# Optimization experiments

Hardware: AMD Instinct MI355X
Metric: run time of the kernel (lower is better)

## Reference

```python
import jax, jax.numpy as jnp
import numpy as np


def gcn_conv(x, W, b, src, dst, dinv_sqrt, n_nodes):
    # PyG GCNConv: h = X W; out_i = sum_j norm_ij * h_j + b, norm = d_i^-1/2 d_j^-1/2
    h = x @ W  # [N, out]
    norm = dinv_sqrt[src] * dinv_sqrt[dst]  # [E]
    msg = h[src] * norm[:, None]  # [E, out]
    out = jax.ops.segment_sum(msg, dst, num_segments=n_nodes)
    return out + b


def setup_inputs() -> dict:
    key = jax.random.key(0)
    ks = jax.random.split(key, 12)
    N, E, G = 50000, 400000, 512
    x = jax.random.normal(ks[0], (N, 3), dtype=jnp.float32)
    edge_index = jax.random.randint(ks[1], (2, E), 0, N, dtype=jnp.int64)
    batch = jnp.sort(jax.random.randint(ks[2], (N,), 0, G, dtype=jnp.int64))
    def lin(k, fin, fout):
        kw, kb = jax.random.split(k)
        s = 1.0 / np.sqrt(fin)
        return (jax.random.uniform(kw, (fin, fout), jnp.float32, -s, s),
                jax.random.uniform(kb, (fout,), jnp.float32, -s, s))
    W1, b1 = lin(ks[3], 3, 100)
    W2, b2 = lin(ks[4], 100, 200)
    W3, b3 = lin(ks[5], 200, 100)
    W4, b4 = lin(ks[6], 100, 1)
    return {"x": x, "edge_index": edge_index, "batch": batch, "num_graphs": G,
            "W1": W1, "b1": b1, "W2": W2, "b2": b2,
            "W3": W3, "b3": b3, "W4": W4, "b4": b4}


def reference(x, edge_index, batch, num_graphs, W1, b1, W2, b2, W3, b3, W4, b4):
    N = x.shape[0]
    loop = jnp.arange(N, dtype=edge_index.dtype)
    src = jnp.concatenate([edge_index[0], loop])  # self-loops added (GCNConv default)
    dst = jnp.concatenate([edge_index[1], loop])
    deg = jax.ops.segment_sum(jnp.ones_like(src, dtype=x.dtype), dst, num_segments=N)
    dinv_sqrt = deg ** -0.5  # deg >= 1 due to self-loops

    h = jax.nn.silu(gcn_conv(x, W1, b1, src, dst, dinv_sqrt, N))
    h = jax.nn.silu(gcn_conv(h, W2, b2, src, dst, dinv_sqrt, N))

    # global_mean_pool over `batch` segments
    sums = jax.ops.segment_sum(h, batch, num_segments=num_graphs)  # [G, 200]
    cnts = jax.ops.segment_sum(jnp.ones((N,), h.dtype), batch, num_segments=num_graphs)
    pooled = sums / jnp.maximum(cnts, 1.0)[:, None]

    h = jax.nn.silu(pooled @ W3 + b3)
    out = h @ W4 + b4  # [G, 1]
    return out.squeeze(-1)
```

## Files before the change

### kernel.cpp

```cpp
#include <hip/hip_runtime.h>
#include <math.h>

#define WF 64

__device__ __forceinline__ float silu_f(float v){ return v / (1.0f + expf(-v)); }

__global__ __launch_bounds__(256) void k_count(const int* __restrict__ dst, int* __restrict__ cnt, int E){
  int e = blockIdx.x*blockDim.x + threadIdx.x;
  if (e < E) atomicAdd(&cnt[dst[e]], 1);
}

__global__ __launch_bounds__(256) void k_scan1(const int* __restrict__ cnt, int* __restrict__ rowstart, int* __restrict__ bsum, int N){
  __shared__ int s[256];
  int tid = threadIdx.x;
  int base = blockIdx.x*2048 + tid*8;
  int loc[8]; int tsum = 0;
#pragma unroll
  for (int j=0;j<8;++j){ int idx=base+j; int v = (idx<N)?cnt[idx]:0; loc[j]=tsum; tsum+=v; }
  s[tid]=tsum; __syncthreads();
  for (int off=1; off<256; off<<=1){
    int v = (tid>=off)? s[tid-off] : 0;
    __syncthreads();
    s[tid] += v;
    __syncthreads();
  }
  int texc = s[tid] - tsum;
  if (tid==255) bsum[blockIdx.x] = s[255];
#pragma unroll
  for (int j=0;j<8;++j){ int idx=base+j; if (idx<N) rowstart[idx] = texc + loc[j]; }
}

__global__ __launch_bounds__(256) void k_scan3(const int* __restrict__ bsum, const int* __restrict__ cnt,
                        const float* __restrict__ x,
                        int* __restrict__ rowstart, int* __restrict__ cursor,
                        float* __restrict__ dinv, float4* __restrict__ dxp,
                        int N, int E, int nb){
  __shared__ int boffs;
  int tid = threadIdx.x;
  int b = (blockIdx.x*blockDim.x) >> 11;
  if (tid < WF){
    int v = (tid < nb && tid < b) ? bsum[tid] : 0;
#pragma unroll
    for (int off=32; off; off>>=1) v += __shfl_down(v, off);
    if (tid==0) boffs = v;
  }
  __syncthreads();
  int idx = blockIdx.x*blockDim.x + tid;
  if (idx < N){
    int v = rowstart[idx] + boffs;
    rowstart[idx]=v; cursor[idx]=v;
    float di = rsqrtf((float)(cnt[idx]+1));
    dinv[idx] = di;
    float4 o;
    o.x = di;
    o.y = di*x[3*idx+0];
    o.z = di*x[3*idx+1];
    o.w = di*x[3*idx+2];
    dxp[idx] = o;
  }
  if (idx==0) rowstart[N]=E;
}

__global__ __launch_bounds__(256) void k_fill(const int* __restrict__ src, const int* __restrict__ dst,
                       int* __restrict__ cursor, int* __restrict__ colsrc, int E){
  int e = blockIdx.x*blockDim.x + threadIdx.x;
  if (e < E){
    int d = dst[e];
    int pos = atomicAdd(&cursor[d], 1);
    colsrc[pos] = src[e];
  }
}

__global__ __launch_bounds__(256) void k_l1(const float4* __restrict__ dxp,
                     const int* __restrict__ rowstart, const int* __restrict__ colsrc,
                     const float* __restrict__ W1, const float* __restrict__ b1,
                     float* __restrict__ h1s, int N){
  __shared__ float w[300];
  __shared__ float bb[100];
  int tid = threadIdx.x;
  for (int t=tid; t<300; t+=blockDim.x) w[t]=W1[t];
  for (int t=tid; t<100; t+=blockDim.x) bb[t]=b1[t];
  __syncthreads();
  int i = blockIdx.x*blockDim.x + tid;
  if (i >= N) return;
  float4 self = dxp[i];
  float di = self.x;
  float sx = self.y, sy = self.z, sz = self.w;
  int jb = rowstart[i], je = rowstart[i+1];
  int j = jb;
  for (; j+3 < je; j += 4){
    float4 r0 = dxp[colsrc[j]];
    float4 r1 = dxp[colsrc[j+1]];
    float4 r2 = dxp[colsrc[j+2]];
    float4 r3 = dxp[colsrc[j+3]];
    sx += (r0.y + r1.y) + (r2.y + r3.y);
    sy += (r0.z + r1.z) + (r2.z + r3.z);
    sz += (r0.w + r1.w) + (r2.w + r3.w);
  }
  for (; j < je; ++j){
    float4 r = dxp[colsrc[j]];
    sx += r.y; sy += r.z; sz += r.w;
  }
  sx*=di; sy*=di; sz*=di;
  float* orow = h1s + (size_t)i*100;
#pragma unroll
  for (int f0=0; f0<100; f0+=4){
    float4 o;
    o.x = silu_f(sx*w[f0+0] + sy*w[100+f0+0] + sz*w[200+f0+0] + bb[f0+0]);
    o.y = silu_f(sx*w[f0+1] + sy*w[100+f0+1] + sz*w[200+f0+1] + bb[f0+1]);
    o.z = silu_f(sx*w[f0+2] + sy*w[100+f0+2] + sz*w[200+f0+2] + bb[f0+2]);
    o.w = silu_f(sx*w[f0+3] + sy*w[100+f0+3] + sz*w[200+f0+3] + bb[f0+3]);
    *(float4*)&orow[f0] = o;
  }
}

__global__ __launch_bounds__(256) void k_agg2(const float* __restrict__ h1s, const int* __restrict__ rowstart,
                       const int* __restrict__ colsrc, const float* __restrict__ dinv,
                       float* __restrict__ a2, int N){
  int node = blockIdx.x*8 + (threadIdx.x >> 5);
  int lane = threadIdx.x & 31;
  if (node >= N) return;
  bool act = lane < 25;
  float di = dinv[node];
  float4 acc = make_float4(0.f,0.f,0.f,0.f);
  if (act){
    float4 v = *(const float4*)(h1s + (size_t)node*100 + lane*4);
    acc.x = di*v.x; acc.y = di*v.y; acc.z = di*v.z; acc.w = di*v.w;
  }
  int jb = rowstart[node], je = rowstart[node+1];
  int j = jb;
  for (; j+1 < je; j += 2){
    int u0 = colsrc[j];   float w0 = dinv[u0];
    int u1 = colsrc[j+1]; float w1 = dinv[u1];
    if (act){
      float4 r0 = *(const float4*)(h1s + (size_t)u0*100 + lane*4);
      float4 r1 = *(const float4*)(h1s + (size_t)u1*100 + lane*4);
      acc.x += w0*r0.x + w1*r1.x;
      acc.y += w0*r0.y + w1*r1.y;
      acc.z += w0*r0.z + w1*r1.z;
      acc.w += w0*r0.w + w1*r1.w;
    }
  }
  if (j < je){
    int u = colsrc[j]; float wv = dinv[u];
    if (act){
      float4 r = *(const float4*)(h1s + (size_t)u*100 + lane*4);
      acc.x += wv*r.x; acc.y += wv*r.y; acc.z += wv*r.z; acc.w += wv*r.w;
    }
  }
  if (act){
    float4 o;
    o.x = di*acc.x; o.y = di*acc.y; o.z = di*acc.z; o.w = di*acc.w;
    *(float4*)(a2 + (size_t)node*100 + lane*4) = o;
  }
}

#define CH 20
__global__ __launch_bounds__(256, 2) void k_mm2(const float* __restrict__ a2, const float* __restrict__ W2,
                      const float* __restrict__ b2, const int* __restrict__ batch,
                      float* __restrict__ pooled, int N){
  __shared__ float aS[CH][260];
  __shared__ float wS[100][48];
  int tid = threadIdx.x;
  int fg = tid & 3;
  int ng = tid >> 2;
  int n0 = blockIdx.x * 256;
  int fb = blockIdx.y;

  for (int idx = tid; idx < 4000; idx += 256){
    int k = idx / 40, f = idx - k*40;
    int g = f / 10, j = f - g*10;
    wS[k][g*12 + j] = W2[(size_t)k*200 + fb*40 + f];
  }

  float acc[4][10];
#pragma unroll
  for (int i=0;i<4;++i)
#pragma unroll
    for (int j=0;j<10;++j) acc[i][j]=0.f;

  int gn = n0 + tid;
  bool inb = (gn < N);
  const float* arow = a2 + (size_t)gn*100;

  for (int kc = 0; kc < 5; ++kc){
    int kt = kc*CH;
    __syncthreads();
#pragma unroll
    for (int c = 0; c < 5; ++c){
      float4 v = make_float4(0.f,0.f,0.f,0.f);
      if (inb) v = *(const float4*)(arow + kt + c*4);
      aS[c*4+0][tid] = v.x;
      aS[c*4+1][tid] = v.y;
      aS[c*4+2][tid] = v.z;
      aS[c*4+3][tid] = v.w;
    }
    __syncthreads();
#pragma unroll
    for (int kl = 0; kl < CH; ++kl){
      float a[4], w[10];
      *(float4*)a = *(const float4*)&aS[kl][ng*4];
      const float* wr = &wS[kt+kl][fg*12];
      *(float4*)&w[0] = *(const float4*)&wr[0];
      *(float4*)&w[4] = *(const float4*)&wr[4];
      *(float2*)&w[8] = *(const float2*)&wr[8];
#pragma unroll
      for (int j=0;j<10;++j){
        float wv = w[j];
#pragma unroll
        for (int i=0;i<4;++i) acc[i][j] += a[i]*wv;
      }
    }
  }

  float* plL = &aS[0][0];
  __syncthreads();
  for (int idx = tid; idx < 640; idx += 256) plL[idx] = 0.f;
  __syncthreads();

  int fbase = fb*40 + fg*10;
  float bias[10];
#pragma unroll
  for (int j=0;j<10;++j) bias[j] = b2[fbase+j];
  int g0 = batch[n0];
  float s[10];
  int gprev = -1;
#pragma unroll
  for (int i=0;i<4;++i){
    int n = n0 + ng*4 + i;
    if (n < N){
      int g = batch[n];
      if (g != gprev){
        if (gprev >= 0){
          int dg = gprev - g0;
          if (dg < 16){
#pragma unroll
            for (int j=0;j<10;++j) atomicAdd(&plL[dg*40 + fg*10 + j], s[j]);
          } else {
#pragma unroll
            for (int j=0;j<10;++j) atomicAdd(&pooled[(size_t)gprev*200 + fbase + j], s[j]);
          }
        }
        gprev = g;
#pragma unroll
        for (int j=0;j<10;++j) s[j] = 0.f;
      }
#pragma unroll
      for (int j=0;j<10;++j) s[j] += silu_f(acc[i][j] + bias[j]);
    }
  }
  if (gprev >= 0){
    int dg = gprev - g0;
    if (dg < 16){
#pragma unroll
      for (int j=0;j<10;++j) atomicAdd(&plL[dg*40 + fg*10 + j], s[j]);
    } else {
#pragma unroll
      for (int j=0;j<10;++j) atomicAdd(&pooled[(size_t)gprev*200 + fbase + j], s[j]);
    }
  }
  __syncthreads();
  for (int idx = tid; idx < 640; idx += 256){
    float v = plL[idx];
    if (v != 0.f){
      int r = idx / 40, f = idx - r*40;
      atomicAdd(&pooled[(size_t)(g0+r)*200 + fb*40 + f], v);
    }
  }
}

__global__ __launch_bounds__(256) void k_head(const float* __restrict__ pooled, const int* __restrict__ batch,
                       const float* __restrict__ W3, const float* __restrict__ b3,
                       const float* __restrict__ W4, const float* __restrict__ b4,
                       float* __restrict__ out, int N){
  __shared__ float pl[200];
  __shared__ float h3[100];
  int g = blockIdx.x; int tid = threadIdx.x;
  int lo=0, hi=N;
  while (lo<hi){ int m=(lo+hi)>>1; if (batch[m] < g) lo=m+1; else hi=m; }
  int s = lo;
  hi=N;
  while (lo<hi){ int m=(lo+hi)>>1; if (batch[m] < g+1) lo=m+1; else hi=m; }
  int e = lo;
  float inv = (e>s) ? 1.0f/(float)(e-s) : 0.0f;
  if (tid < 200) pl[tid] = pooled[(size_t)g*200 + tid] * inv;
  __syncthreads();
  if (tid < 100){
    float acc = b3[tid];
    for (int k=0;k<200;++k) acc += pl[k]*W3[k*100+tid];
    h3[tid] = silu_f(acc);
  }
  __syncthreads();
  if (tid < WF){
    float p = 0.f;
    if (tid < 100)      p  = h3[tid]     * W4[tid];
    if (tid + 64 < 100) p += h3[tid+64]  * W4[tid+64];
#pragma unroll
    for (int off=32; off; off>>=1) p += __shfl_down(p, off);
    if (tid==0) out[g] = p + b4[0];
  }
}

extern "C" void kernel_launch(void* const* d_in, const int* in_sizes, int n_in,
                              void* d_out, int out_size, void* d_ws, size_t ws_size,
                              hipStream_t stream){
  const float* x  = (const float*)d_in[0];
  const int*   ei = (const int*)  d_in[1];
  const int* batch= (const int*)  d_in[2];
  const float* W1 = (const float*)d_in[4];
  const float* b1 = (const float*)d_in[5];
  const float* W2 = (const float*)d_in[6];
  const float* b2 = (const float*)d_in[7];
  const float* W3 = (const float*)d_in[8];
  const float* b3 = (const float*)d_in[9];
  const float* W4 = (const float*)d_in[10];
  const float* b4 = (const float*)d_in[11];
  float* out = (float*)d_out;

  int N = in_sizes[0]/3;
  int E = in_sizes[1]/2;
  int G = out_size;
  const int* src = ei;
  const int* dst = ei + E;

  char* base = (char*)d_ws; size_t off = 0;
  auto alloc = [&](size_t bytes)->void*{
    void* p = base + off;
    off = (off + bytes + 255) & ~(size_t)255;
    return p;
  };
  int*   cnt      = (int*)  alloc((size_t)N*4);
  float* pooled   = (float*)alloc((size_t)G*200*4);
  size_t zbytes   = off;
  int*   rowstart = (int*)  alloc((size_t)(N+1)*4);
  int*   cursor   = (int*)  alloc((size_t)N*4);
  int*   bsum     = (int*)  alloc(4096);
  int*   colsrc   = (int*)  alloc((size_t)E*4);
  float* dinv     = (float*)alloc((size_t)N*4);
  float4* dxp     = (float4*)alloc((size_t)N*16);
  float* h1s      = (float*)alloc((size_t)N*100*4);
  float* a2       = (float*)alloc((size_t)N*100*4);
  (void)ws_size; (void)n_in;

  hipMemsetAsync(base, 0, zbytes, stream);
  int gE = (E+255)/256;
  k_count<<<gE,256,0,stream>>>(dst, cnt, E);
  int nb = (N+2047)/2048;
  k_scan1<<<nb,256,0,stream>>>(cnt, rowstart, bsum, N);
  k_scan3<<<(N+255)/256,256,0,stream>>>(bsum, cnt, x, rowstart, cursor, dinv, dxp, N, E, nb);
  k_fill<<<gE,256,0,stream>>>(src, dst, cursor, colsrc, E);
  k_l1<<<(N+255)/256,256,0,stream>>>(dxp, rowstart, colsrc, W1, b1, h1s, N);
  k_agg2<<<(N+7)/8,256,0,stream>>>(h1s, rowstart, colsrc, dinv, a2, N);
  dim3 gmm((N+255)/256, 5);
  k_mm2<<<gmm,256,0,stream>>>(a2, W2, b2, batch, pooled, N);
  k_head<<<G,256,0,stream>>>(pooled, batch, W3, b3, W4, b4, out, N);
}
```

Before: 184.2 us.

## Shrink mm2 node tile to 128 and stream W2 chunks per k-step

Reworks the layer-2 matmul+pool kernel to use 128-node tiles with 2 rows per thread instead of 256 nodes with 4. W2 is now loaded per 20-row k-chunk rather than all at once, which cuts shared memory and registers. The grid is transposed so the 5 feature blocks sharing a node tile launch next to each other, which should improve L2 reuse of a2. The aim is more blocks and higher occupancy, at the cost of less register reuse per W load and more loads and syncs.

```diff
diff --git a/kernel.cpp b/kernel.cpp
--- a/kernel.cpp
+++ b/kernel.cpp
@@ -156,66 +156,62 @@
 }
 
 #define CH 20
-__global__ __launch_bounds__(256, 2) void k_mm2(const float* __restrict__ a2, const float* __restrict__ W2,
+__global__ __launch_bounds__(256) void k_mm2(const float* __restrict__ a2, const float* __restrict__ W2,
                       const float* __restrict__ b2, const int* __restrict__ batch,
                       float* __restrict__ pooled, int N){
-  __shared__ float aS[CH][260];
-  __shared__ float wS[100][48];
+  __shared__ float aS[CH][132];
+  __shared__ float wS[CH][48];
   int tid = threadIdx.x;
   int fg = tid & 3;
   int ng = tid >> 2;
-  int n0 = blockIdx.x * 256;
-  int fb = blockIdx.y;
-
-  for (int idx = tid; idx < 4000; idx += 256){
-    int k = idx / 40, f = idx - k*40;
-    int g = f / 10, j = f - g*10;
-    wS[k][g*12 + j] = W2[(size_t)k*200 + fb*40 + f];
-  }
-
-  float acc[4][10];
-#pragma unroll
-  for (int i=0;i<4;++i)
+  int fb = blockIdx.x;
+  int n0 = blockIdx.y * 128;
+
+  float acc[2][10];
+#pragma unroll
+  for (int i=0;i<2;++i)
 #pragma unroll
     for (int j=0;j<10;++j) acc[i][j]=0.f;
-
-  int gn = n0 + tid;
-  bool inb = (gn < N);
-  const float* arow = a2 + (size_t)gn*100;
 
   for (int kc = 0; kc < 5; ++kc){
     int kt = kc*CH;
     __syncthreads();
-#pragma unroll
-    for (int c = 0; c < 5; ++c){
+    for (int idx = tid; idx < 640; idx += 256){
+      int n = idx / 5, q = idx - n*5;
+      int gn = n0 + n;
       float4 v = make_float4(0.f,0.f,0.f,0.f);
-      if (inb) v = *(const float4*)(arow + kt + c*4);
-      aS[c*4+0][tid] = v.x;
-      aS[c*4+1][tid] = v.y;
-      aS[c*4+2][tid] = v.z;
-      aS[c*4+3][tid] = v.w;
+      if (gn < N) v = *(const float4*)(a2 + (size_t)gn*100 + kt + q*4);
+      aS[q*4+0][n] = v.x;
+      aS[q*4+1][n] = v.y;
+      aS[q*4+2][n] = v.z;
+      aS[q*4+3][n] = v.w;
+    }
+    for (int idx = tid; idx < 800; idx += 256){
+      int kl = idx / 40, f = idx - kl*40;
+      int g = f / 10, j = f - g*10;
+      wS[kl][g*12 + j] = W2[(size_t)(kt+kl)*200 + fb*40 + f];
     }
     __syncthreads();
 #pragma unroll
     for (int kl = 0; kl < CH; ++kl){
-      float a[4], w[10];
-      *(float4*)a = *(const float4*)&aS[kl][ng*4];
-      const float* wr = &wS[kt+kl][fg*12];
+      float a[2], w[10];
+      *(float2*)a = *(const float2*)&aS[kl][ng*2];
+      const float* wr = &wS[kl][fg*12];
       *(float4*)&w[0] = *(const float4*)&wr[0];
       *(float4*)&w[4] = *(const float4*)&wr[4];
       *(float2*)&w[8] = *(const float2*)&wr[8];
 #pragma unroll
       for (int j=0;j<10;++j){
         float wv = w[j];
-#pragma unroll
-        for (int i=0;i<4;++i) acc[i][j] += a[i]*wv;
+        acc[0][j] += a[0]*wv;
+        acc[1][j] += a[1]*wv;
       }
     }
   }
 
   float* plL = &aS[0][0];
   __syncthreads();
-  for (int idx = tid; idx < 640; idx += 256) plL[idx] = 0.f;
+  for (int idx = tid; idx < 320; idx += 256) plL[idx] = 0.f;
   __syncthreads();
 
   int fbase = fb*40 + fg*10;
@@ -226,14 +222,14 @@
   float s[10];
   int gprev = -1;
 #pragma unroll
-  for (int i=0;i<4;++i){
-    int n = n0 + ng*4 + i;
+  for (int i=0;i<2;++i){
+    int n = n0 + ng*2 + i;
     if (n < N){
       int g = batch[n];
       if (g != gprev){
         if (gprev >= 0){
           int dg = gprev - g0;
-          if (dg < 16){
+          if (dg < 8){
 #pragma unroll
             for (int j=0;j<10;++j) atomicAdd(&plL[dg*40 + fg*10 + j], s[j]);
           } else {
@@ -251,7 +247,7 @@
   }
   if (gprev >= 0){
     int dg = gprev - g0;
-    if (dg < 16){
+    if (dg < 8){
 #pragma unroll
       for (int j=0;j<10;++j) atomicAdd(&plL[dg*40 + fg*10 + j], s[j]);
     } else {
@@ -260,7 +256,7 @@
     }
   }
   __syncthreads();
-  for (int idx = tid; idx < 640; idx += 256){
+  for (int idx = tid; idx < 320; idx += 256){
     float v = plL[idx];
     if (v != 0.f){
       int r = idx / 40, f = idx - r*40;
@@ -351,7 +347,7 @@
   k_fill<<<gE,256,0,stream>>>(src, dst, cursor, colsrc, E);
   k_l1<<<(N+255)/256,256,0,stream>>>(dxp, rowstart, colsrc, W1, b1, h1s, N);
   k_agg2<<<(N+7)/8,256,0,stream>>>(h1s, rowstart, colsrc, dinv, a2, N);
-  dim3 gmm((N+255)/256, 5);
+  dim3 gmm(5, (N+127)/128);
   k_mm2<<<gmm,256,0,stream>>>(a2, W2, b2, batch, pooled, N);
   k_head<<<G,256,0,stream>>>(pooled, batch, W3, b3, W4, b4, out, N);
 }
```

Measured after the change: 199.7 us. +8.4%, slower.
